# Kernel tuning notes

Hardware: AMD Instinct MI355X
Metric: run time of the kernel (lower is better)

Reference implementation:

```python
import jax, jax.numpy as jnp
import numpy as np

N = 1536        # nodes in batch
E = 24576       # directed edges (avg in-degree 16)
H_DIM = 128     # hidden_dim
D = 1280        # input_dim (esm embedding size)
K_HOPS = 2
RATIO = 0.5     # node-drop pooling keep ratio
NEG = -1e9

def _leaky(v):
    return jnp.where(v > 0, v, 0.2 * v)

def setup_inputs():
    key = jax.random.key(0)
    ks = jax.random.split(key, 11)
    x = jax.random.normal(ks[0], (N, H_DIM), jnp.float32)
    x_orig = jax.random.normal(ks[1], (N, D), jnp.float32) * 0.1
    edge_index = jax.random.randint(ks[2], (2, E), 0, N, dtype=jnp.int32)
    batch = jnp.zeros((N,), jnp.int32)
    W1 = jax.random.normal(ks[3], (H_DIM, D), jnp.float32) / np.sqrt(H_DIM).astype(np.float32)
    a_src1 = jax.random.normal(ks[4], (D,), jnp.float32) / np.sqrt(D).astype(np.float32)
    a_dst1 = jax.random.normal(ks[5], (D,), jnp.float32) / np.sqrt(D).astype(np.float32)
    b1 = jnp.zeros((D,), jnp.float32)
    w2 = jax.random.normal(ks[6], (D,), jnp.float32) / np.sqrt(D).astype(np.float32)
    a_s2 = jax.random.normal(ks[7], (), jnp.float32)
    a_d2 = jax.random.normal(ks[8], (), jnp.float32)
    b2 = jnp.zeros((), jnp.float32)
    return {"x": x, "x_orig": x_orig, "edge_index": edge_index, "batch": batch,
            "W1": W1, "a_src1": a_src1, "a_dst1": a_dst1, "b1": b1,
            "w2": w2, "a_s2": a_s2, "a_d2": a_d2, "b2": b2}

def _forward(x, x_orig, edge_index, batch, W1, a_src1, a_dst1, b1, w2, a_s2, a_d2, b2):
    n = x.shape[0]
    src, tgt = edge_index[0], edge_index[1]
    sl = jnp.arange(n, dtype=src.dtype)
    src2 = jnp.concatenate([src, sl])   # PyG GATConv adds self-loops
    tgt2 = jnp.concatenate([tgt, sl])

    # ---- conv1: GATConv(hidden_dim -> input_dim, heads=1) on full graph ----
    h = x @ W1                                          # [N, D]
    e = _leaky((h @ a_src1)[src2] + (h @ a_dst1)[tgt2])  # [E+N]
    mx = jax.ops.segment_max(e, tgt2, num_segments=n)
    ex = jnp.exp(e - mx[tgt2])
    den = jax.ops.segment_sum(ex, tgt2, num_segments=n)
    alpha = ex / den[tgt2]
    x_gat = jax.ops.segment_sum(alpha[:, None] * h[src2], tgt2, num_segments=n) + b1

    # ---- batched k-hop ego masks (flow source->target, center included) ----
    A = jnp.zeros((n, n), jnp.float32).at[src, tgt].set(1.0)
    M = jnp.eye(n, dtype=jnp.float32)
    for _ in range(K_HOPS):
        M = jnp.minimum(M + M @ A.T, 1.0)
    Mb = M > 0                                          # [N_ego, N_node]

    # ---- pooling scorer GAT(D->1) on x_sub = x_gat[v] * x_orig[u] ----
    # h2[v,u] = sum_d x_gat[v,d] * x_orig[u,d] * w2[d]
    H2 = (x_gat * w2) @ x_orig.T                        # [N_ego, N_node]
    hs, ht = H2[:, src2], H2[:, tgt2]                   # [N_ego, E+N]
    valid = Mb[:, src2] & Mb[:, tgt2]
    e2 = jnp.where(valid, _leaky(a_s2 * hs + a_d2 * ht), NEG)

    def row(e_row, hs_row):  # attention softmax + aggregate within one ego
        m = jax.ops.segment_max(e_row, tgt2, num_segments=n)
        w = jnp.exp(e_row - m[tgt2])
        d = jax.ops.segment_sum(w, tgt2, num_segments=n)
        nu = jax.ops.segment_sum(w * hs_row, tgt2, num_segments=n)
        return nu / jnp.maximum(d, 1e-12)
    score = jax.vmap(row)(e2, hs) + b2                  # [N_ego, N_node]

    # ---- node-drop pooling: keep top ceil(RATIO*|ego|) nodes per ego ----
    size = jnp.sum(Mb, axis=1).astype(jnp.float32)
    k_keep = jnp.ceil(RATIO * size).astype(jnp.int32)
    score_m = jnp.where(Mb, score, NEG)
    order = jnp.argsort(-score_m, axis=1)
    rank = jnp.argsort(order, axis=1)
    keep = (rank < k_keep[:, None]) & Mb
    out = jnp.where(keep, jax.nn.sigmoid(score), 0.0)   # padded score matrix
    return out, keep

def reference(x, x_orig, edge_index, batch, W1, a_src1, a_dst1, b1, w2, a_s2, a_d2, b2):
    return _forward(x, x_orig, edge_index, batch, W1, a_src1, a_dst1, b1, w2, a_s2, a_d2, b2)
```

## Files before the change

### kernel.cpp

```cpp
#include <hip/hip_runtime.h>
#include <math.h>

#define N 1536
#define E 24576
#define HD 128
#define D 1280
#define NW 24
#define RT 16
#define LDK 40
#define KSP 4
#define KSL 320

typedef unsigned long long u64;
typedef unsigned short u16;
typedef unsigned int u32;
typedef __attribute__((ext_vector_type(8))) short bf16x8;
typedef __attribute__((ext_vector_type(4))) float f32x4;

__device__ __forceinline__ double lrelu(double v){ return v > 0.0 ? v : 0.2*v; }

__device__ __forceinline__ double fexp(double x){
    double n = __builtin_rint(x * 1.4426950408889634);
    double r = __builtin_fma(-n, 0.6931471805599453, x);
    r = __builtin_fma(-n, 2.3190468138462996e-17, r);
    double p = 2.505210838544172e-8;
    p = __builtin_fma(p, r, 2.755731922398589e-7);
    p = __builtin_fma(p, r, 2.7557319223985893e-6);
    p = __builtin_fma(p, r, 2.48015873015873e-5);
    p = __builtin_fma(p, r, 1.984126984126984e-4);
    p = __builtin_fma(p, r, 1.3888888888888889e-3);
    p = __builtin_fma(p, r, 8.333333333333333e-3);
    p = __builtin_fma(p, r, 4.1666666666666664e-2);
    p = __builtin_fma(p, r, 1.6666666666666666e-1);
    p = __builtin_fma(p, r, 0.5);
    p = __builtin_fma(p, r, 1.0);
    p = __builtin_fma(p, r, 1.0);
    long long ni = (long long)n;
    double s = __longlong_as_double((u64)(ni + 1023) << 52);
    return (x < -700.0) ? 0.0 : p * s;
}

__device__ __forceinline__ float fexpf_(float x){
    float n = __builtin_rintf(x * 1.44269504f);
    float r = __builtin_fmaf(-n, 0.693359375f, x);
    r = __builtin_fmaf(-n, -2.12194440e-4f, r);
    float p = 1.9841270e-4f;
    p = __builtin_fmaf(p, r, 1.3888889e-3f);
    p = __builtin_fmaf(p, r, 8.3333333e-3f);
    p = __builtin_fmaf(p, r, 4.1666667e-2f);
    p = __builtin_fmaf(p, r, 1.6666667e-1f);
    p = __builtin_fmaf(p, r, 0.5f);
    p = __builtin_fmaf(p, r, 1.0f);
    p = __builtin_fmaf(p, r, 1.0f);
    int ni = (int)n;
    float s = __uint_as_float((u32)(ni + 127) << 23);
    return p * s;
}

__device__ __forceinline__ void bsplit(float f, u16& h, u16& l){
    unsigned u = __float_as_uint(f);
    unsigned hr = (u + 0x7fffu + ((u>>16)&1u)) >> 16;
    h = (u16)hr;
    float hf = __uint_as_float(hr << 16);
    float r = f - hf;
    unsigned u2 = __float_as_uint(r);
    l = (u16)((u2 + 0x7fffu + ((u2>>16)&1u)) >> 16);
}

__global__ void k_deg_in(const int* __restrict__ ei, u64* __restrict__ IN, int* __restrict__ deg){
    int idx = blockIdx.x*blockDim.x + threadIdx.x;
    if (idx < E){
        int s = ei[idx], t = ei[E+idx];
        atomicOr(&IN[(size_t)t*NW + (s>>6)], 1ULL << (s&63));
        atomicAdd(&deg[t], 1);
    } else if (idx < E+N){
        atomicAdd(&deg[idx-E], 1);
    }
}

__global__ void k_scan(const int* __restrict__ deg, int* __restrict__ coff, int* __restrict__ cursor){
    __shared__ int ls[256];
    int tid = threadIdx.x;
    int v[6]; int s = 0;
    for (int u=0; u<6; u++){ v[u] = s; s += deg[tid*6+u]; }
    ls[tid] = s; __syncthreads();
    for (int d=1; d<256; d<<=1){
        int t2 = (tid>=d) ? ls[tid-d] : 0;
        __syncthreads();
        ls[tid] += t2;
        __syncthreads();
    }
    int base = (tid>0) ? ls[tid-1] : 0;
    for (int u=0; u<6; u++){
        int o = base + v[u];
        coff[tid*6+u] = o; cursor[tid*6+u] = o;
    }
    if (tid==255) coff[N] = ls[255];
}

__global__ void k_fill(const int* __restrict__ ei, int* __restrict__ cursor, u16* __restrict__ csr_src){
    int idx = blockIdx.x*blockDim.x + threadIdx.x;
    if (idx < E){
        int s = ei[idx], t = ei[E+idx];
        int p = atomicAdd(&cursor[t], 1);
        csr_src[p] = (u16)s;
    } else if (idx < E+N){
        int t = idx - E;
        int p = atomicAdd(&cursor[t], 1);
        csr_src[p] = (u16)t;
    }
}

__global__ void k_mrow(const u64* __restrict__ IN, u64* __restrict__ Mb,
                       u16* __restrict__ cols, int* __restrict__ cnt){
    int i = blockIdx.x, ln = threadIdx.x;
    __shared__ u64 m1[NW];
    __shared__ int scn[64];
    __shared__ u16 lst[N];
    u64 b = 0;
    if (ln < NW){
        b = IN[(size_t)i*NW + ln];
        if ((i>>6) == ln) b |= 1ULL << (i&63);
        m1[ln] = b;
    }
    int pc = (ln < NW) ? __popcll(b) : 0;
    scn[ln] = pc; __syncthreads();
    for (int d=1; d<64; d<<=1){
        int v = (ln>=d) ? scn[ln-d] : 0;
        __syncthreads();
        scn[ln] += v;
        __syncthreads();
    }
    {
        int idx = scn[ln] - pc;
        u64 bb = b;
        while (bb){
            int k = __ffsll((unsigned long long)bb) - 1;
            bb &= bb - 1;
            lst[idx++] = (u16)(ln*64 + k);
        }
    }
    __syncthreads();
    int nn = scn[63];
    u64 R0 = b, R1 = 0, R2 = 0, R3 = 0;
    int u = 0;
    if (ln < NW){
        for (; u+3 < nn; u += 4){
            R0 |= IN[(size_t)lst[u  ]*NW + ln];
            R1 |= IN[(size_t)lst[u+1]*NW + ln];
            R2 |= IN[(size_t)lst[u+2]*NW + ln];
            R3 |= IN[(size_t)lst[u+3]*NW + ln];
        }
        for (; u < nn; u++) R0 |= IN[(size_t)lst[u]*NW + ln];
    }
    u64 R = (R0 | R1) | (R2 | R3);
    if (ln < NW) Mb[(size_t)i*NW + ln] = R;
    __syncthreads();
    pc = (ln < NW) ? __popcll(R) : 0;
    scn[ln] = pc; __syncthreads();
    for (int d=1; d<64; d<<=1){
        int v = (ln>=d) ? scn[ln-d] : 0;
        __syncthreads();
        scn[ln] += v;
        __syncthreads();
    }
    if (ln == 63) cnt[i] = scn[63];
    int idx = scn[ln] - pc;
    u64 bb = R;
    while (bb){
        int k = __ffsll((unsigned long long)bb) - 1;
        bb &= bb - 1;
        cols[(size_t)i*N + idx++] = (u16)(ln*64 + k);
    }
}

__global__ void k_h(const float* __restrict__ x, const float* __restrict__ W1, float* __restrict__ h32){
    int rb = blockIdx.y*RT, tid = threadIdx.x;
    int col = blockIdx.x*256 + tid;
    __shared__ float xL[RT*HD];
    for (int u=tid; u<RT*HD; u+=256) xL[u] = x[(size_t)rb*HD + u];
    __syncthreads();
    float acc[RT];
    #pragma unroll
    for (int r=0; r<RT; r++) acc[r] = 0.0f;
    const float* wp = &W1[col];
    #pragma unroll 4
    for (int k=0; k<HD; k++){
        float w = wp[(size_t)k*D];
        #pragma unroll
        for (int r=0; r<RT; r++) acc[r] = __builtin_fmaf(w, xL[r*HD + k], acc[r]);
    }
    #pragma unroll
    for (int r=0; r<RT; r++) h32[(size_t)(rb+r)*D + col] = acc[r];
}

__global__ void k_hv(const float* __restrict__ h32, const float* __restrict__ as1,
                     const float* __restrict__ ad1, double* __restrict__ hs1, double* __restrict__ hd1){
    int i = blockIdx.x, tid = threadIdx.x;
    __shared__ double ra[256], rb[256];
    double a = 0, b = 0;
    for (int d=tid; d<D; d+=256){
        double hv = (double)h32[(size_t)i*D + d];
        a += hv * (double)as1[d];
        b += hv * (double)ad1[d];
    }
    ra[tid] = a; rb[tid] = b; __syncthreads();
    for (int s=128; s>0; s>>=1){
        if (tid < s){ ra[tid] += ra[tid+s]; rb[tid] += rb[tid+s]; }
        __syncthreads();
    }
    if (tid == 0){ hs1[i] = ra[0]; hd1[i] = rb[0]; }
}

__global__ void k_split_x(const float* __restrict__ xo, u16* __restrict__ Xhi, u16* __restrict__ Xlo){
    int idx = (blockIdx.x*256 + threadIdx.x)*4;
    float4 v = *(const float4*)&xo[idx];
    ushort4 h, l;
    bsplit(v.x, h.x, l.x); bsplit(v.y, h.y, l.y);
    bsplit(v.z, h.z, l.z); bsplit(v.w, h.w, l.w);
    *(ushort4*)&Xhi[idx] = h;
    *(ushort4*)&Xlo[idx] = l;
}

__global__ void k_gat(const int* __restrict__ coff, const u16* __restrict__ csr_src,
                      const double* __restrict__ hs1, const double* __restrict__ hd1,
                      const float* __restrict__ h32,
                      const float* __restrict__ b1, const float* __restrict__ w2,
                      u16* __restrict__ Ghi, u16* __restrict__ Glo){
    int t = blockIdx.x, tid = threadIdx.x;
    int o0 = coff[t], o1 = coff[t+1], dg = o1 - o0;
    __shared__ double red[256];
    __shared__ float als[256];
    __shared__ int ssrc[256];
    __shared__ double DD;
    double hdt = hd1[t];
    double dsum = 0.0;
    for (int j=tid; j<dg; j+=256){
        int s = csr_src[o0+j];
        double e = lrelu(hs1[s] + hdt);
        dsum += fexp(e);
    }
    red[tid] = dsum; __syncthreads();
    for (int step=128; step>0; step>>=1){
        if (tid < step) red[tid] += red[tid+step];
        __syncthreads();
    }
    if (tid == 0) DD = red[0];
    __syncthreads();
    double Dv = DD;
    float acc[5] = {0,0,0,0,0};
    for (int base=0; base<dg; base+=256){
        int j = base + tid;
        if (j < dg){
            int s = csr_src[o0+j];
            double e = lrelu(hs1[s] + hdt);
            als[tid] = (float)(fexp(e)/Dv); ssrc[tid] = s;
        }
        __syncthreads();
        int lim = min(256, dg-base);
        for (int u=0; u<lim; u+=2){
            float a0 = als[u];
            int s0 = ssrc[u];
            bool h1 = (u+1 < lim);
            float a1 = h1 ? als[u+1] : 0.0f;
            int s1 = h1 ? ssrc[u+1] : s0;
            const float* hp0 = &h32[(size_t)s0*D];
            const float* hp1 = &h32[(size_t)s1*D];
            #pragma unroll
            for (int q=0; q<5; q++)
                acc[q] = __builtin_fmaf(a1, hp1[tid + 256*q],
                         __builtin_fmaf(a0, hp0[tid + 256*q], acc[q]));
        }
        __syncthreads();
    }
    #pragma unroll
    for (int q=0; q<5; q++){
        int d = tid + 256*q;
        float g = (acc[q] + b1[d]) * w2[d];
        u16 gh, gl;
        bsplit(g, gh, gl);
        Ghi[(size_t)t*D + d] = gh;
        Glo[(size_t)t*D + d] = gl;
    }
}

__global__ __launch_bounds__(512, 4)
void k_h2mm(const u16* __restrict__ Ghi, const u16* __restrict__ Glo,
            const u16* __restrict__ Xhi, const u16* __restrict__ Xlo,
            float* __restrict__ Hp){
    __shared__ u16 As_hi[128*LDK], As_lo[128*LDK], Bs_hi[128*LDK], Bs_lo[128*LDK];
    int tid = threadIdx.x;
    int ks = blockIdx.x & (KSP-1);
    int tile = blockIdx.x >> 2;
    int bm = tile / 12, bn = tile % 12;
    int r0 = tid >> 2;
    int kc = (tid & 3) * 8;
    int k0 = ks * KSL;
    size_t baseA = (size_t)(bm*128 + r0)*D + k0 + kc;
    size_t baseB = (size_t)(bn*128 + r0)*D + k0 + kc;
    int w = tid >> 6, L = tid & 63;
    int l16 = L & 15, qd = L >> 4;
    int wm = (w & 1)*64, wn = (w >> 1)*32;
    f32x4 acc[4][2];
    #pragma unroll
    for (int a=0; a<4; a++)
        #pragma unroll
        for (int b=0; b<2; b++) acc[a][b] = (f32x4){0.f,0.f,0.f,0.f};

    for (int kb = 0; kb < KSL; kb += 32){
        uint4 ah = *(const uint4*)&Ghi[baseA + kb];
        uint4 al = *(const uint4*)&Glo[baseA + kb];
        uint4 bh = *(const uint4*)&Xhi[baseB + kb];
        uint4 bl = *(const uint4*)&Xlo[baseB + kb];
        __syncthreads();
        *(uint4*)&As_hi[r0*LDK + kc] = ah;
        *(uint4*)&As_lo[r0*LDK + kc] = al;
        *(uint4*)&Bs_hi[r0*LDK + kc] = bh;
        *(uint4*)&Bs_lo[r0*LDK + kc] = bl;
        __syncthreads();
        bf16x8 ahi[4], alo[4];
        #pragma unroll
        for (int tm=0; tm<4; tm++){
            ahi[tm] = *(const bf16x8*)&As_hi[(wm + tm*16 + l16)*LDK + qd*8];
            alo[tm] = *(const bf16x8*)&As_lo[(wm + tm*16 + l16)*LDK + qd*8];
        }
        #pragma unroll
        for (int tn=0; tn<2; tn++){
            bf16x8 bhf = *(const bf16x8*)&Bs_hi[(wn + tn*16 + l16)*LDK + qd*8];
            bf16x8 blf = *(const bf16x8*)&Bs_lo[(wn + tn*16 + l16)*LDK + qd*8];
            #pragma unroll
            for (int tm=0; tm<4; tm++){
                acc[tm][tn] = __builtin_amdgcn_mfma_f32_16x16x32_bf16(ahi[tm], bhf, acc[tm][tn], 0, 0, 0);
                acc[tm][tn] = __builtin_amdgcn_mfma_f32_16x16x32_bf16(alo[tm], bhf, acc[tm][tn], 0, 0, 0);
                acc[tm][tn] = __builtin_amdgcn_mfma_f32_16x16x32_bf16(ahi[tm], blf, acc[tm][tn], 0, 0, 0);
            }
        }
    }
    float* HO = Hp + (size_t)ks*N*N;
    #pragma unroll
    for (int tm=0; tm<4; tm++){
        int rbase = bm*128 + wm + tm*16 + qd*4;
        #pragma unroll
        for (int tn=0; tn<2; tn++){
            int cg = bn*128 + wn + tn*16 + l16;
            #pragma unroll
            for (int reg=0; reg<4; reg++)
                HO[(size_t)(rbase+reg)*N + cg] = acc[tm][tn][reg];
        }
    }
}

__global__ void k_score_rank(const float* __restrict__ Hp, const u64* __restrict__ Mb,
                             const u16* __restrict__ cols, const int* __restrict__ cnt,
                             const int* __restrict__ coff, const u16* __restrict__ csr_src,
                             const float* __restrict__ pas2, const float* __restrict__ pad2,
                             const float* __restrict__ pb2, float* __restrict__ out){
    int i = blockIdx.x, tid = threadIdx.x;
    __shared__ __align__(16) float HL[N];
    __shared__ u64 MbL[NW];
    __shared__ u16 clL[N];
    __shared__ u64 KL[N];
    float* keepO = out + (size_t)N*N;
    {
        const float4* P0 = (const float4*)(Hp + (size_t)i*N);
        const float4* P1 = (const float4*)(Hp + (size_t)N*N   + (size_t)i*N);
        const float4* P2 = (const float4*)(Hp + (size_t)2*N*N + (size_t)i*N);
        const float4* P3 = (const float4*)(Hp + (size_t)3*N*N + (size_t)i*N);
        float4* H4 = (float4*)HL;
        for (int u=tid; u<N/4; u+=256){
            float4 a=P0[u], b=P1[u], c=P2[u], d=P3[u];
            float4 r;
            r.x = (a.x+b.x)+(c.x+d.x);
            r.y = (a.y+b.y)+(c.y+d.y);
            r.z = (a.z+b.z)+(c.z+d.z);
            r.w = (a.w+b.w)+(c.w+d.w);
            H4[u] = r;
        }
    }
    if (tid < NW) MbL[tid] = Mb[(size_t)i*NW + tid];
    __syncthreads();
    float as2 = pas2[0], ad2 = pad2[0];
    double b2 = (double)pb2[0];
    int c0 = cnt[i];
    for (int c=tid; c<c0; c+=256){
        int t = cols[(size_t)i*N + c];
        float ht = HL[t];
        float zd = ad2 * ht;
        int o0 = coff[t], o1 = coff[t+1];
        double den = 0.0, nu = 0.0;
        int p = o0;
        for (; p+7 < o1; p += 8){
            int s[8]; float h[8]; float wv[8];
            #pragma unroll
            for (int q=0; q<8; q++) s[q] = csr_src[p+q];
            #pragma unroll
            for (int q=0; q<8; q++) h[q] = HL[s[q]];
            #pragma unroll
            for (int q=0; q<8; q++){
                bool v = (MbL[s[q]>>6] >> (s[q]&63)) & 1ULL;
                float z = __builtin_fmaf(as2, h[q], zd);
                float e = z > 0.f ? z : 0.2f*z;
                e = fminf(fmaxf(e, -80.f), 80.f);
                wv[q] = v ? fexpf_(e) : 0.0f;
            }
            #pragma unroll
            for (int q=0; q<8; q++){
                den += (double)wv[q];
                nu  += (double)(wv[q]*h[q]);
            }
        }
        for (; p < o1; p++){
            int s = csr_src[p];
            bool v = (MbL[s>>6] >> (s&63)) & 1ULL;
            float hs = HL[s];
            float z = __builtin_fmaf(as2, hs, zd);
            float e = z > 0.0f ? z : 0.2f*z;
            e = fminf(fmaxf(e, -80.0f), 80.0f);
            float w = v ? fexpf_(e) : 0.0f;
            den += (double)w;
            nu  += (double)(w * hs);
        }
        float sf = (float)(nu / fmax(den, 1e-12) + b2);
        clL[c] = (u16)t;
        u32 kb = __float_as_uint(sf);
        kb = (kb & 0x80000000u) ? ~kb : (kb | 0x80000000u);
        KL[c] = ((u64)kb << 16) | (u32)(1535 - t);
    }
    __syncthreads();
    for (int d=tid; d<N; d+=256) HL[d] = 0.0f;
    __syncthreads();
    int k = (c0 + 1) >> 1;
    for (int p=tid; p<c0; p+=256){
        u64 Kp = KL[p];
        int r = 0;
        for (int q=0; q<c0; q++) r += (int)(KL[q] > Kp);
        if (r < k){
            u32 kb = (u32)(Kp >> 16);
            u32 orig = (kb & 0x80000000u) ? (kb & 0x7fffffffu) : ~kb;
            float sf = __uint_as_float(orig);
            HL[clL[p]] = 1.0f/(1.0f + fexpf_(fminf(fmaxf(-sf,-80.f),80.f)));
        }
    }
    __syncthreads();
    {
        const float4* H4 = (const float4*)HL;
        float4* O0 = (float4*)(out   + (size_t)i*N);
        float4* O1 = (float4*)(keepO + (size_t)i*N);
        for (int u=tid; u<N/4; u+=256){
            float4 s = H4[u];
            float4 kk;
            kk.x = (s.x > 0.0f) ? 1.0f : 0.0f;
            kk.y = (s.y > 0.0f) ? 1.0f : 0.0f;
            kk.z = (s.z > 0.0f) ? 1.0f : 0.0f;
            kk.w = (s.w > 0.0f) ? 1.0f : 0.0f;
            O0[u] = s;
            O1[u] = kk;
        }
    }
}

extern "C" void kernel_launch(void* const* d_in, const int* in_sizes, int n_in,
                              void* d_out, int out_size, void* d_ws, size_t ws_size,
                              hipStream_t stream){
    const float* x   = (const float*)d_in[0];
    const float* xo  = (const float*)d_in[1];
    const int*   ei  = (const int*)  d_in[2];
    const float* W1  = (const float*)d_in[4];
    const float* as1 = (const float*)d_in[5];
    const float* ad1 = (const float*)d_in[6];
    const float* b1  = (const float*)d_in[7];
    const float* w2  = (const float*)d_in[8];
    const float* as2 = (const float*)d_in[9];
    const float* ad2 = (const float*)d_in[10];
    const float* b2  = (const float*)d_in[11];
    float* out = (float*)d_out;

    char* w = (char*)d_ws;
    size_t o = 0;
    auto alloc = [&](size_t b)->char*{ char* r = w + o; o = (o + b + 255) & ~(size_t)255; return r; };

    float*  h32   = (float*) alloc((size_t)N*D*4);
    float*  Hp    = (float*) alloc((size_t)KSP*N*N*4);
    u16*    Ghi   = (u16*)   alloc((size_t)N*D*2);
    u16*    Glo   = (u16*)   alloc((size_t)N*D*2);
    u16*    Xhi   = (u16*)   alloc((size_t)N*D*2);
    u16*    Xlo   = (u16*)   alloc((size_t)N*D*2);
    u64*    IN    = (u64*)   alloc((size_t)N*NW*8);
    int*    deg   = (int*)   alloc((size_t)N*4);
    u64*    Mb    = (u64*)   alloc((size_t)N*NW*8);
    double* hs1   = (double*)alloc((size_t)N*8);
    double* hd1   = (double*)alloc((size_t)N*8);
    int*    coff  = (int*)   alloc((size_t)(N+1)*4);
    int*    cursor= (int*)   alloc((size_t)N*4);
    u16*    csr   = (u16*)   alloc((size_t)(E+N)*2);
    u16*    cols  = (u16*)   alloc((size_t)N*N*2);
    int*    cnt   = (int*)   alloc((size_t)N*4);

    hipMemsetAsync(IN, 0, (size_t)N*NW*8 + (size_t)N*4, stream);

    k_deg_in <<<(E+N+255)/256, 256, 0, stream>>>(ei, IN, deg);
    k_scan   <<<1, 256, 0, stream>>>(deg, coff, cursor);
    k_fill   <<<(E+N+255)/256, 256, 0, stream>>>(ei, cursor, csr);
    k_split_x<<<(N*D)/(256*4), 256, 0, stream>>>(xo, Xhi, Xlo);
    k_mrow   <<<N, 64, 0, stream>>>(IN, Mb, cols, cnt);
    k_h      <<<dim3(D/256, N/RT), 256, 0, stream>>>(x, W1, h32);
    k_hv     <<<N, 256, 0, stream>>>(h32, as1, ad1, hs1, hd1);
    k_gat    <<<N, 256, 0, stream>>>(coff, csr, hs1, hd1, h32, b1, w2, Ghi, Glo);
    k_h2mm   <<<144*KSP, 512, 0, stream>>>(Ghi, Glo, Xhi, Xlo, Hp);
    k_score_rank<<<N, 256, 0, stream>>>(Hp, Mb, cols, cnt, coff, csr, as2, ad2, b2, out);
}
```

Baseline: 219.8 us.

## Replace quadratic rank counting with radix-select threshold for top-k selection

The per-ego top-k selection used to compare each key against every other key, which is O(c0^2) shared-memory reads per block. It now runs a byte-wise radix select over the 48-bit keys: six passes that build a 256-bin histogram with shared atomics, a wavefront prefix scan, and a narrowing of the prefix to find the k-th largest key as a threshold. Elements with keys at or above the threshold are kept. Because keys are unique (the node index is packed into the low bits), the selected set should be unchanged, but the change adds several block syncs and atomic contention per pass.

```diff
diff --git a/kernel.cpp b/kernel.cpp
--- a/kernel.cpp
+++ b/kernel.cpp
@@ -360,6 +360,9 @@
     __shared__ u64 MbL[NW];
     __shared__ u16 clL[N];
     __shared__ u64 KL[N];
+    __shared__ int hist[256];
+    __shared__ u64 sPrefix;
+    __shared__ int sKK;
     float* keepO = out + (size_t)N*N;
     {
         const float4* P0 = (const float4*)(Hp + (size_t)i*N);
@@ -382,6 +385,7 @@
     float as2 = pas2[0], ad2 = pad2[0];
     double b2 = (double)pb2[0];
     int c0 = cnt[i];
+    c0 = min(max(c0, 0), N);
     for (int c=tid; c<c0; c+=256){
         int t = cols[(size_t)i*N + c];
         float ht = HL[t];
@@ -428,13 +432,48 @@
     }
     __syncthreads();
     for (int d=tid; d<N; d+=256) HL[d] = 0.0f;
-    __syncthreads();
     int k = (c0 + 1) >> 1;
+    if (tid == 0){ sPrefix = 0; sKK = k; }
+    #pragma unroll 1
+    for (int shift = 40; shift >= 0; shift -= 8){
+        hist[tid] = 0;
+        __syncthreads();
+        u64 pref = sPrefix;
+        int kkr = sKK;
+        for (int c=tid; c<c0; c+=256){
+            u64 key = KL[c];
+            if ((key >> (shift+8)) == (pref >> (shift+8)))
+                atomicAdd(&hist[(int)((key>>shift)&255)], 1);
+        }
+        __syncthreads();
+        if (tid < 64){
+            int Lx = tid;
+            int b0 = hist[4*Lx], b1v = hist[4*Lx+1], b2v = hist[4*Lx+2], b3v = hist[4*Lx+3];
+            int tot = ((b0 + b1v) + (b2v + b3v));
+            int run = tot;
+            #pragma unroll
+            for (int d=1; d<64; d<<=1){
+                int o = __shfl_down(run, d);
+                if (Lx + d < 64) run += o;
+            }
+            int after = run - tot;
+            int s3 = b3v + after, s2 = b2v + s3, s1 = b1v + s2, s0 = b0 + s1;
+            int dg = -1, rem = 0;
+            if (s0 >= kkr && s1 < kkr){ dg = 4*Lx;   rem = kkr - s1; }
+            else if (s1 >= kkr && s2 < kkr){ dg = 4*Lx+1; rem = kkr - s2; }
+            else if (s2 >= kkr && s3 < kkr){ dg = 4*Lx+2; rem = kkr - s3; }
+            else if (s3 >= kkr && after < kkr){ dg = 4*Lx+3; rem = kkr - after; }
+            if (dg >= 0){
+                sPrefix = pref | ((u64)(u32)dg << shift);
+                sKK = rem;
+            }
+        }
+        __syncthreads();
+    }
+    u64 T = sPrefix;
     for (int p=tid; p<c0; p+=256){
         u64 Kp = KL[p];
-        int r = 0;
-        for (int q=0; q<c0; q++) r += (int)(KL[q] > Kp);
-        if (r < k){
+        if (Kp >= T){
             u32 kb = (u32)(Kp >> 16);
             u32 orig = (kb & 0x80000000u) ? (kb & 0x7fffffffu) : ~kb;
             float sf = __uint_as_float(orig);
```

Result: faster. 209.2 us (-4.8%).
